# Performance work log

Measured on AMD Instinct MI355X. Metric: run time of the kernel, lower is better.

The kernel has to match this reference:

```python
import jax, jax.numpy as jnp
import numpy as np

N_NODES = 100000
N_EDGES = 1600000
HID = 128
HEADS = 8
DK = HID // HEADS
N_LAYERS = 4
IN_DIM = 32
N_CLASSES = 16


def _ln(x, g, b, eps=1e-5):
    mu = x.mean(-1, keepdims=True)
    var = x.var(-1, keepdims=True)
    return (x - mu) / jnp.sqrt(var + eps) * g + b


def setup_inputs() -> dict:
    key = jax.random.key(0)
    ks = jax.random.split(key, 24)
    s = 0.05
    inp = {
        'feat': jax.random.randint(ks[0], (N_NODES,), 0, IN_DIM, dtype=jnp.int32),
        'edge_src': jax.random.randint(ks[1], (N_EDGES,), 0, N_NODES, dtype=jnp.int32),
        'edge_dst': jnp.sort(jax.random.randint(ks[2], (N_EDGES,), 0, N_NODES, dtype=jnp.int32)),
        'emb': jax.random.normal(ks[3], (IN_DIM, HID), jnp.float32) * s,
        'Wq': jax.random.normal(ks[4], (N_LAYERS, HID, HID), jnp.float32) * s,
        'Wk': jax.random.normal(ks[5], (N_LAYERS, HID, HID), jnp.float32) * s,
        'Wv': jax.random.normal(ks[6], (N_LAYERS, HID, HID), jnp.float32) * s,
        'Wo': jax.random.normal(ks[7], (N_LAYERS, HID, HID), jnp.float32) * s,
        'bo': jnp.zeros((N_LAYERS, HID), jnp.float32),
        'ln1_g': jnp.ones((N_LAYERS, HID), jnp.float32),
        'ln1_b': jnp.zeros((N_LAYERS, HID), jnp.float32),
        'W1': jax.random.normal(ks[8], (N_LAYERS, HID, 2 * HID), jnp.float32) * s,
        'b1': jnp.zeros((N_LAYERS, 2 * HID), jnp.float32),
        'W2': jax.random.normal(ks[9], (N_LAYERS, 2 * HID, HID), jnp.float32) * s,
        'b2': jnp.zeros((N_LAYERS, HID), jnp.float32),
        'ln2_g': jnp.ones((N_LAYERS, HID), jnp.float32),
        'ln2_b': jnp.zeros((N_LAYERS, HID), jnp.float32),
        'mW0': jax.random.normal(ks[10], (HID, HID // 2), jnp.float32) * s,
        'mb0': jnp.zeros((HID // 2,), jnp.float32),
        'mW1': jax.random.normal(ks[11], (HID // 2, HID // 4), jnp.float32) * s,
        'mb1': jnp.zeros((HID // 4,), jnp.float32),
        'mW2': jax.random.normal(ks[12], (HID // 4, N_CLASSES), jnp.float32) * s,
        'mb2': jnp.zeros((N_CLASSES,), jnp.float32),
    }
    return inp


def reference(feat, edge_src, edge_dst, emb, Wq, Wk, Wv, Wo, bo, ln1_g, ln1_b,
              W1, b1, W2, b2, ln2_g, ln2_b, mW0, mb0, mW1, mb1, mW2, mb2):
    N = feat.shape[0]
    h = emb[feat]  # [N, HID] embedding gather
    inv_sqrt_dk = jnp.float32(1.0 / np.sqrt(DK))
    for l in range(Wq.shape[0]):
        h_in1 = h
        q = (h @ Wq[l]).reshape(N, HEADS, DK)
        k = (h @ Wk[l]).reshape(N, HEADS, DK)
        v = (h @ Wv[l]).reshape(N, HEADS, DK)
        # per-edge scores: K[src] . Q[dst], scaled, clipped, exponentiated
        sc = jnp.einsum('ehd,ehd->eh', k[edge_src], q[edge_dst]) * inv_sqrt_dk
        sc = jnp.exp(jnp.clip(sc, -5.0, 5.0))  # [E, HEADS]
        wV = jax.ops.segment_sum(sc[:, :, None] * v[edge_src], edge_dst, num_segments=N)
        z = jax.ops.segment_sum(sc, edge_dst, num_segments=N)
        attn = (wV / (z[:, :, None] + 1e-6)).reshape(N, HID)
        h = h_in1 + (attn @ Wo[l] + bo[l])  # residual + O proj
        h = _ln(h, ln1_g[l], ln1_b[l])
        h_in2 = h
        f = jax.nn.relu(h @ W1[l] + b1[l]) @ W2[l] + b2[l]
        h = _ln(h_in2 + f, ln2_g[l], ln2_b[l])
    # MLPReadout: HID -> HID/2 -> HID/4 -> n_classes
    h = jax.nn.relu(h @ mW0 + mb0)
    h = jax.nn.relu(h @ mW1 + mb1)
    return h @ mW2 + mb2
```

## Files before the change

### kernel.cpp

```cpp
#include <hip/hip_runtime.h>
#include <hip/hip_fp16.h>

#define HID 128
#define N_LAYERS 4
#define IN_DIM 32
#define N_CLASSES 16

typedef _Float16 f16x8 __attribute__((ext_vector_type(8)));
typedef float f32x2 __attribute__((ext_vector_type(2)));
typedef __attribute__((ext_vector_type(4))) float f32x4;
typedef unsigned int uint_t;

#if defined(__has_builtin)
#if __has_builtin(__builtin_amdgcn_cvt_pk_f32_fp8)
#define HAVE_CVT_FP8 1
#endif
#if __has_builtin(__builtin_amdgcn_cvt_pk_fp8_f32)
#define HAVE_ENC_FP8 1
#endif
#endif

__device__ __forceinline__ unsigned short f2bf(float f) {
    unsigned int u = __float_as_uint(f);
    return (unsigned short)((u + 0x7FFFu + ((u >> 16) & 1u)) >> 16);
}
__device__ __forceinline__ float2 up16(uint_t u) {
    __half2 h = *(__half2*)&u;
    return __half22float2(h);
}

__device__ __forceinline__ unsigned char f2e4m3(float f) {
    unsigned int u = __float_as_uint(f);
    unsigned char s = (unsigned char)((u >> 24) & 0x80u);
    unsigned int a = u & 0x7FFFFFFFu;
    if (a >= 0x43E00000u) return s | 0x7Eu;
    int exp = (int)(a >> 23) - 127;
    if (exp < -6) {
        int m = (int)rintf(__uint_as_float(a) * 512.f);
        return s | (unsigned char)m;
    }
    unsigned int lsb = (a >> 20) & 1u;
    a += 0x7FFFFu + lsb;
    int e8 = ((int)(a >> 23) - 127) + 7;
    unsigned int m8 = (a >> 20) & 7u;
    return s | (unsigned char)((e8 << 3) | (int)m8);
}
__device__ __forceinline__ float e4m32f(unsigned int b) {
    unsigned int s = (b & 0x80u) << 24;
    unsigned int E = (b >> 3) & 15u, m = b & 7u;
    if (E == 0) {
        float v = (float)m * 0.001953125f;
        return __uint_as_float(__float_as_uint(v) | s);
    }
    return __uint_as_float(s | ((E + 120u) << 23) | (m << 20));
}
__device__ __forceinline__ unsigned char enc8(float v) {
#ifdef HAVE_ENC_FP8
    int r = __builtin_amdgcn_cvt_pk_fp8_f32(v, v, 0, false);
    return (unsigned char)(r & 0xFF);
#else
    return f2e4m3(v);
#endif
}
__device__ __forceinline__ void dec8v(uint_t u, f32x2* o) {
#ifdef HAVE_CVT_FP8
    o[0] = __builtin_amdgcn_cvt_pk_f32_fp8(u, false);
    o[1] = __builtin_amdgcn_cvt_pk_f32_fp8(u, true);
#else
    o[0] = (f32x2){e4m32f(u & 255u), e4m32f((u >> 8) & 255u)};
    o[1] = (f32x2){e4m32f((u >> 16) & 255u), e4m32f(u >> 24)};
#endif
}

__device__ __forceinline__ int frag_off(int row, int c) {
    return ((c >> 5) << 10) + (((c >> 3) & 3) << 8) + (row << 4) + ((c & 7) << 1);
}

__global__ void detect_kernel(const unsigned int* __restrict__ ln1g, int* __restrict__ flag) {
    if (threadIdx.x == 0 && blockIdx.x == 0)
        *flag = (ln1g[0] == 0x3F800000u) ? 0 : 1;
}

#define NSM 11
struct SArgs {
    const void* src[NSM];
    float*      dst[NSM];
    int         cnt[NSM];
};

__global__ void conv_kernel(SArgs args, const int* __restrict__ flag) {
    int p = blockIdx.y;
    int n = args.cnt[p];
    int base = (blockIdx.x * 256 + threadIdx.x) * 4;
    if (base >= n) return;
    float* dst = args.dst[p];
    if (*flag) {
        const unsigned short* s = (const unsigned short*)args.src[p];
        #pragma unroll
        for (int j = 0; j < 4; ++j)
            dst[base + j] = __uint_as_float(((unsigned int)s[base + j]) << 16);
    } else {
        const float* s = (const float*)args.src[p];
        *(float4*)&dst[base] = *(const float4*)&s[base];
    }
}

#define NW 27
struct WArgs {
    const void* src[NW];
    int         soff[NW];
    _Float16*   dst[NW];
    int         K[NW];
    int         M[NW];
    int         mode[NW];
};

__global__ void wconv_kernel(WArgs a, const int* __restrict__ flag) {
    int p = blockIdx.y;
    int K = a.K[p], M = a.M[p], mode = a.mode[p];
    int idx = blockIdx.x * 256 + threadIdx.x;
    if (idx >= K * M) return;
    int k = idx / M, m = idx % M;
    float v;
    if (*flag)
        v = __uint_as_float(((unsigned int)((const unsigned short*)a.src[p])[a.soff[p] + idx]) << 16);
    else
        v = ((const float*)a.src[p])[a.soff[p] + idx];
    size_t off;
    if (mode == 0) {
        off = (size_t)m * K + k;
    } else {
        int ht, k2;
        if (mode == 1) { ht = m >> 5; k2 = k; }
        else           { ht = ((k >> 7) << 2) + (m >> 5); k2 = k & 127; }
        int frag = (((k2 >> 5) * 2 + ((m >> 4) & 1)) << 6) + (((k2 >> 3) & 3) << 4) + (m & 15);
        off = (size_t)ht * 4096 + frag * 8 + (k & 7);
    }
    a.dst[p][off] = (_Float16)v;
}

__global__ void csr_kernel(const int* __restrict__ dst, int* __restrict__ row_start,
                           int N, int E) {
    int n = blockIdx.x * 256 + threadIdx.x;
    if (n > N) return;
    int lo = 0, hi = E;
    while (lo < hi) {
        int mid = (lo + hi) >> 1;
        if (dst[mid] < n) lo = mid + 1; else hi = mid;
    }
    row_start[n] = lo;
}

__global__ void embed_kernel(const int* __restrict__ feat, const float* __restrict__ emb,
                             _Float16* __restrict__ h, int N) {
    int idx = blockIdx.x * 256 + threadIdx.x;
    if (idx >= N * 16) return;
    int n  = idx >> 4;
    int c8 = idx & 15;
    int f = feat[n];
    const float* s = &emb[(size_t)f * HID + c8 * 8];
    float4 a = *(const float4*)s;
    float4 b = *(const float4*)(s + 4);
    f16x8 o;
    o[0] = (_Float16)a.x; o[1] = (_Float16)a.y; o[2] = (_Float16)a.z; o[3] = (_Float16)a.w;
    o[4] = (_Float16)b.x; o[5] = (_Float16)b.y; o[6] = (_Float16)b.z; o[7] = (_Float16)b.w;
    *(f16x8*)&h[(size_t)n * HID + c8 * 8] = o;
}

__launch_bounds__(256)
__global__ void mfma_gemm_qkv(const _Float16* __restrict__ Ain,
                              const _Float16* __restrict__ Bt,
                              _Float16* __restrict__ q16, unsigned char* __restrict__ kvp8) {
    __shared__ __align__(16) char As[16384];
    __shared__ __align__(16) char Bs[49152];

    const int t    = threadIdx.x;
    const int w    = t >> 6;
    const int l    = t & 63;
    const int quad = l >> 4;
    const int lc   = l & 15;
    const int row0 = blockIdx.x * 64;
    const int mbase = blockIdx.y * 192;

    char* Aw = As + (w << 12);

    #pragma unroll
    for (int i = 0; i < 4; ++i) {
        int idx = i * 64 + l;
        int row = idx >> 4, g = idx & 15;
        uint4 v = *(const uint4*)(Ain + (size_t)(row0 + w * 16 + row) * 128 + g * 8);
        *(uint4*)(Aw + ((g >> 2) << 10) + ((g & 3) << 8) + (row << 4)) = v;
    }
    {
        const uint4* Bsrc = (const uint4*)(Bt + (size_t)(mbase / 32) * 4096);
        #pragma unroll
        for (int i = 0; i < 12; ++i) {
            int idx = t + i * 256;
            *(uint4*)&Bs[idx * 16] = Bsrc[idx];
        }
    }
    __syncthreads();

    f32x4 acc[12];
    #pragma unroll
    for (int i = 0; i < 12; ++i) acc[i] = (f32x4){0.f, 0.f, 0.f, 0.f};

    #pragma unroll
    for (int kk = 0; kk < 4; ++kk) {
        f16x8 af = *(const f16x8*)(Aw + (kk << 10) + (quad << 8) + (lc << 4));
        #pragma unroll
        for (int i = 0; i < 12; ++i) {
            f16x8 bf = *(const f16x8*)(Bs + (i >> 1) * 8192 +
                                       ((kk * 2 + (i & 1)) << 10) + (quad << 8) + (lc << 4));
            acc[i] = __builtin_amdgcn_mfma_f32_16x16x32_f16(af, bf, acc[i], 0, 0, 0);
        }
    }

    #pragma unroll
    for (int r = 0; r < 4; ++r) {
        int row = row0 + w * 16 + quad * 4 + r;
        #pragma unroll
        for (int i = 0; i < 12; ++i) {
            float v = acc[i][r];
            int gc = mbase + i * 16 + lc;
            if (gc < 128)      q16[(size_t)row * 128 + gc] = (_Float16)v;
            else if (gc < 256) kvp8[(size_t)row * 256 + (gc - 128)] = enc8(v);
            else               kvp8[(size_t)row * 256 + 128 + (gc - 256)] = enc8(v);
        }
    }
}

template<int NEXTM, bool RMODE>
__launch_bounds__(256, 3)
__global__ void layer_fused(_Float16* __restrict__ h,
                            const _Float16* __restrict__ Wo, const _Float16* __restrict__ W1,
                            const _Float16* __restrict__ W2,
                            const _Float16* __restrict__ Wn, const float* __restrict__ bn,
                            const float* __restrict__ bo,  const float* __restrict__ l1g,
                            const float* __restrict__ l1b, const float* __restrict__ b1,
                            const float* __restrict__ b2,  const float* __restrict__ l2g,
                            const float* __restrict__ l2b,
                            _Float16* __restrict__ q16,
                            const uint_t* __restrict__ kvin, unsigned char* __restrict__ kvout,
                            const int* __restrict__ esrc, const int* __restrict__ rows,
                            int N) {
    constexpr int NHT = NEXTM / 32;
    __shared__ __align__(16) char bufA[16384];
    __shared__ __align__(16) char bufH[16384];
    __shared__ __align__(16) char bufB[16384];

    const int t = threadIdx.x, w = t >> 6, l = t & 63;
    const int quad = l >> 4, lc = l & 15;
    const int row0 = blockIdx.x * 64;
    char* Aw = bufA + (w << 12);
    char* Hw = bufH + (w << 12);

    auto ISSUE = [&](const _Float16* src, int bsel) {
        char* d = bufB + bsel * 8192 + w * 2048;
        const char* g = (const char*)src + w * 2048 + l * 16;
        __builtin_amdgcn_global_load_lds(
            (const __attribute__((address_space(1))) unsigned int*)g,
            (__attribute__((address_space(3))) unsigned int*)d, 16, 0, 0);
        __builtin_amdgcn_global_load_lds(
            (const __attribute__((address_space(1))) unsigned int*)(g + 1024),
            (__attribute__((address_space(3))) unsigned int*)(d + 1024), 16, 0, 0);
    };
    auto MF2 = [&](const char* Ar, int bsel, f32x4* ac) {
        const char* B = bufB + bsel * 8192;
        #pragma unroll
        for (int kk = 0; kk < 4; ++kk) {
            f16x8 af = *(const f16x8*)(Ar + (kk << 10) + (quad << 8) + (lc << 4));
            #pragma unroll
            for (int i = 0; i < 2; ++i) {
                f16x8 bf = *(const f16x8*)(B + ((kk * 2 + i) << 10) + (quad << 8) + (lc << 4));
                ac[i] = __builtin_amdgcn_mfma_f32_16x16x32_f16(af, bf, ac[i], 0, 0, 0);
            }
        }
    };

    ISSUE(Wo, 0);

    _Float16 resv[4][8];
    #pragma unroll
    for (int r = 0; r < 4; ++r) {
        int row = row0 + w * 16 + quad * 4 + r;
        #pragma unroll
        for (int j = 0; j < 8; ++j)
            resv[r][j] = h[(size_t)row * 128 + j * 16 + lc];
    }

    {
        const int head = l & 7;
        const int rsub = l >> 3;
        #pragma unroll
        for (int task = 0; task < 2; ++task) {
            const int rr   = rsub + task * 8;
            const int node = row0 + w * 16 + rr;
            f16x8 o0, o1;
            #pragma unroll
            for (int j = 0; j < 8; ++j) { o0[j] = (_Float16)0; o1[j] = (_Float16)0; }
            if (node < N) {
                f32x2 qh[8];
                {
                    const uint4* qp = (const uint4*)(q16 + (size_t)node * HID + head * 16);
                    uint4 q0 = qp[0], q1 = qp[1];
                    uint_t qs[8] = {q0.x, q0.y, q0.z, q0.w, q1.x, q1.y, q1.z, q1.w};
                    #pragma unroll
                    for (int i = 0; i < 8; ++i) {
                        float2 f = up16(qs[i]);
                        qh[i] = (f32x2){f.x * 0.25f, f.y * 0.25f};
                    }
                }
                int e0 = rows[node], e1 = rows[node + 1];
                f32x2 wv[8];
                #pragma unroll
                for (int i = 0; i < 8; ++i) wv[i] = (f32x2){0.f, 0.f};
                float z = 0.f;

                uint4 ka = {0,0,0,0}, va = {0,0,0,0}, kc = {0,0,0,0}, vc = {0,0,0,0};
                bool oka = e0 < e1, okc = e0 + 1 < e1;
                if (oka) {
                    int sa = esrc[e0];
                    int sc = okc ? esrc[e0 + 1] : sa;
                    ka = *(const uint4*)(kvin + (size_t)sa * 64 + head * 4);
                    va = *(const uint4*)(kvin + (size_t)sa * 64 + 32 + head * 4);
                    kc = *(const uint4*)(kvin + (size_t)sc * 64 + head * 4);
                    vc = *(const uint4*)(kvin + (size_t)sc * 64 + 32 + head * 4);
                }
                for (int e = e0; e < e1; e += 2) {
                    uint4 cka = ka, cva = va, ckc = kc, cvc = vc;
                    bool coka = oka, cokc = okc;
                    int en = e + 2;
                    oka = en < e1; okc = en + 1 < e1;
                    if (oka) {
                        int sa = esrc[en];
                        int sc = okc ? esrc[en + 1] : sa;
                        ka = *(const uint4*)(kvin + (size_t)sa * 64 + head * 4);
                        va = *(const uint4*)(kvin + (size_t)sa * 64 + 32 + head * 4);
                        kc = *(const uint4*)(kvin + (size_t)sc * 64 + head * 4);
                        vc = *(const uint4*)(kvin + (size_t)sc * 64 + 32 + head * 4);
                    }
                    f32x2 k2a[8], k2c[8];
                    dec8v(cka.x, k2a); dec8v(cka.y, k2a + 2); dec8v(cka.z, k2a + 4); dec8v(cka.w, k2a + 6);
                    dec8v(ckc.x, k2c); dec8v(ckc.y, k2c + 2); dec8v(ckc.z, k2c + 4); dec8v(ckc.w, k2c + 6);
                    f32x2 da2 = (f32x2){0.f, 0.f}, dc2 = (f32x2){0.f, 0.f};
                    #pragma unroll
                    for (int j = 0; j < 8; ++j) { da2 += qh[j] * k2a[j]; dc2 += qh[j] * k2c[j]; }
                    float da = da2.x + da2.y, dc = dc2.x + dc2.y;
                    float sa2 = coka ? __expf(fminf(fmaxf(da, -5.f), 5.f)) : 0.f;
                    float sc2 = cokc ? __expf(fminf(fmaxf(dc, -5.f), 5.f)) : 0.f;

                    f32x2 v2a[8], v2c[8];
                    dec8v(cva.x, v2a); dec8v(cva.y, v2a + 2); dec8v(cva.z, v2a + 4); dec8v(cva.w, v2a + 6);
                    dec8v(cvc.x, v2c); dec8v(cvc.y, v2c + 2); dec8v(cvc.z, v2c + 4); dec8v(cvc.w, v2c + 6);
                    f32x2 pa = (f32x2){sa2, sa2}, pc = (f32x2){sc2, sc2};
                    #pragma unroll
                    for (int j = 0; j < 8; ++j) { wv[j] += pa * v2a[j]; wv[j] += pc * v2c[j]; }
                    z += sa2 + sc2;
                }
                float inv = 1.f / (z + 1e-6f);
                #pragma unroll
                for (int i = 0; i < 4; ++i) {
                    o0[2*i]   = (_Float16)(wv[i].x * inv);
                    o0[2*i+1] = (_Float16)(wv[i].y * inv);
                    o1[2*i]   = (_Float16)(wv[4+i].x * inv);
                    o1[2*i+1] = (_Float16)(wv[4+i].y * inv);
                }
            }
            *(f16x8*)(Aw + frag_off(rr, head * 16))     = o0;
            *(f16x8*)(Aw + frag_off(rr, head * 16 + 8)) = o1;
        }
    }

    __syncthreads();
    int bb = 0;

    f32x4 acc[8];
    #pragma unroll
    for (int i = 0; i < 8; ++i) acc[i] = (f32x4){0.f, 0.f, 0.f, 0.f};
    #pragma unroll
    for (int c = 0; c < 4; ++c) {
        ISSUE(c < 3 ? Wo + (c + 1) * 4096 : W1, bb ^ 1);
        MF2(Aw, bb, acc + c * 2);
        __syncthreads();
        bb ^= 1;
    }

    {
        float gv[8], bv[8], bb8[8];
        #pragma unroll
        for (int j = 0; j < 8; ++j) {
            int col = j * 16 + lc;
            gv[j] = l1g[col]; bv[j] = l1b[col]; bb8[j] = bo[col];
        }
        #pragma unroll
        for (int r = 0; r < 4; ++r) {
            float v[8];
            float s = 0.f, ss = 0.f;
            #pragma unroll
            for (int j = 0; j < 8; ++j) {
                v[j] = acc[j][r] + bb8[j] + (float)resv[r][j];
                s += v[j]; ss += v[j] * v[j];
            }
            #pragma unroll
            for (int m = 1; m <= 8; m <<= 1) { s += __shfl_xor(s, m); ss += __shfl_xor(ss, m); }
            float mu   = s * (1.f / 128.f);
            float rstd = rsqrtf(ss * (1.f / 128.f) - mu * mu + 1e-5f);
            #pragma unroll
            for (int j = 0; j < 8; ++j) {
                float o = (v[j] - mu) * rstd * gv[j] + bv[j];
                *(_Float16*)(Hw + frag_off(quad * 4 + r, j * 16 + lc)) = (_Float16)o;
            }
        }
    }

    f32x4 acc3[8];
    #pragma unroll
    for (int i = 0; i < 8; ++i) acc3[i] = (f32x4){0.f, 0.f, 0.f, 0.f};
    #pragma unroll
    for (int hh = 0; hh < 2; ++hh) {
        #pragma unroll
        for (int j = 0; j < 4; ++j) {
            ISSUE(j < 3 ? W1 + (hh * 4 + j + 1) * 4096 : W2 + (hh * 4) * 4096, bb ^ 1);
            f32x4 a2[2];
            a2[0] = (f32x4){0.f, 0.f, 0.f, 0.f};
            a2[1] = (f32x4){0.f, 0.f, 0.f, 0.f};
            MF2(Hw, bb, a2);
            #pragma unroll
            for (int r = 0; r < 4; ++r) {
                #pragma unroll
                for (int i2 = 0; i2 < 2; ++i2) {
                    float v = a2[i2][r] + b1[(hh * 4 + j) * 32 + i2 * 16 + lc];
                    v = fmaxf(v, 0.f);
                    *(_Float16*)(Aw + frag_off(quad * 4 + r, j * 32 + i2 * 16 + lc)) = (_Float16)v;
                }
            }
            __syncthreads();
            bb ^= 1;
        }
        #pragma unroll
        for (int j = 0; j < 4; ++j) {
            const _Float16* nxt;
            if (j < 3)          nxt = W2 + (hh * 4 + j + 1) * 4096;
            else if (hh == 0)   nxt = W1 + 4 * 4096;
            else                nxt = Wn;
            ISSUE(nxt, bb ^ 1);
            MF2(Aw, bb, acc3 + j * 2);
            __syncthreads();
            bb ^= 1;
        }
    }

    f16x8 ov[4];
    {
        float gv[8], bv[8], bb8[8];
        #pragma unroll
        for (int j = 0; j < 8; ++j) {
            int col = j * 16 + lc;
            gv[j] = l2g[col]; bv[j] = l2b[col]; bb8[j] = b2[col];
        }
        #pragma unroll
        for (int r = 0; r < 4; ++r) {
            float v[8];
            float s = 0.f, ss = 0.f;
            #pragma unroll
            for (int j = 0; j < 8; ++j) {
                float res = (float)*(const _Float16*)(Hw + frag_off(quad * 4 + r, j * 16 + lc));
                v[j] = acc3[j][r] + bb8[j] + res;
                s += v[j]; ss += v[j] * v[j];
            }
            #pragma unroll
            for (int m = 1; m <= 8; m <<= 1) { s += __shfl_xor(s, m); ss += __shfl_xor(ss, m); }
            float mu   = s * (1.f / 128.f);
            float rstd = rsqrtf(ss * (1.f / 128.f) - mu * mu + 1e-5f);
            #pragma unroll
            for (int j = 0; j < 8; ++j) {
                float o = (v[j] - mu) * rstd * gv[j] + bv[j];
                ov[r][j] = (_Float16)o;
                *(_Float16*)(Aw + frag_off(quad * 4 + r, j * 16 + lc)) = (_Float16)o;
            }
        }
    }

    auto storeP = [&](int p, const f32x4* pf) {
        #pragma unroll
        for (int r = 0; r < 4; ++r) {
            int row = row0 + w * 16 + quad * 4 + r;
            #pragma unroll
            for (int i2 = 0; i2 < 2; ++i2) {
                int gc = p * 32 + i2 * 16 + lc;
                float v = pf[i2][r];
                if (RMODE) {
                    v += bn[gc];
                    v = fmaxf(v, 0.f);
                    q16[(size_t)row * 64 + gc] = (_Float16)v;
                } else {
                    if (gc < 128)      q16[(size_t)row * 128 + gc] = (_Float16)v;
                    else if (gc < 256) kvout[(size_t)row * 256 + (gc - 128)] = enc8(v);
                    else               kvout[(size_t)row * 256 + 128 + (gc - 256)] = enc8(v);
                }
            }
        }
    };

    f32x4 pf[2];
    #pragma unroll
    for (int c = 0; c < NHT; ++c) {
        if (c + 1 < NHT) ISSUE(Wn + (c + 1) * 4096, bb ^ 1);
        if (c == 0) {
            #pragma unroll
            for (int r = 0; r < 4; ++r) {
                int row = row0 + w * 16 + quad * 4 + r;
                #pragma unroll
                for (int j = 0; j < 8; ++j)
                    h[(size_t)row * 128 + j * 16 + lc] = ov[r][j];
            }
        } else {
            storeP(c - 1, pf);
        }
        f32x4 a4[2];
        a4[0] = (f32x4){0.f, 0.f, 0.f, 0.f};
        a4[1] = (f32x4){0.f, 0.f, 0.f, 0.f};
        MF2(Aw, bb, a4);
        if (c + 1 < NHT) __syncthreads();
        bb ^= 1;
        pf[0] = a4[0]; pf[1] = a4[1];
    }
    storeP(NHT - 1, pf);
}

__launch_bounds__(256)
__global__ void readout_tail(const _Float16* __restrict__ r0,
                             const _Float16* __restrict__ w1t, const float* __restrict__ b1_,
                             const _Float16* __restrict__ w2t, const float* __restrict__ b2_,
                             void* __restrict__ outp, const int* __restrict__ flag, int N) {
    constexpr int SA = 144;
    constexpr int SR = 80;
    __shared__ __align__(16) char bufA[64 * SA];
    __shared__ __align__(16) char bufR[64 * SR];

    const int t    = threadIdx.x;
    const int w    = t >> 6;
    const int l    = t & 63;
    const int quad = l >> 4;
    const int lc   = l & 15;
    const int row0 = blockIdx.x * 64;

    #pragma unroll
    for (int i = 0; i < 2; ++i) {
        int idx = t + i * 256;
        int r = idx >> 3, u = idx & 7;
        *(uint4*)&bufA[r * SA + u * 16] = *(const uint4*)(r0 + (size_t)(row0 + r) * 64 + u * 8);
    }
    __syncthreads();

    f32x4 acc[2];
    acc[0] = (f32x4){0.f, 0.f, 0.f, 0.f};
    acc[1] = (f32x4){0.f, 0.f, 0.f, 0.f};
    #pragma unroll
    for (int kk = 0; kk < 2; ++kk) {
        f16x8 af = *(const f16x8*)&bufA[(w * 16 + lc) * SA + kk * 64 + quad * 16];
        #pragma unroll
        for (int i = 0; i < 2; ++i) {
            f16x8 bf = *(const f16x8*)(w1t + (size_t)(i * 16 + lc) * 64 + kk * 32 + quad * 8);
            acc[i] = __builtin_amdgcn_mfma_f32_16x16x32_f16(af, bf, acc[i], 0, 0, 0);
        }
    }
    #pragma unroll
    for (int r = 0; r < 4; ++r) {
        int lrow = (w * 16 + quad * 4 + r) * SR;
        #pragma unroll
        for (int i = 0; i < 2; ++i) {
            float v = acc[i][r] + b1_[i * 16 + lc];
            v = fmaxf(v, 0.f);
            *(_Float16*)&bufR[lrow + (i * 16 + lc) * 2] = (_Float16)v;
        }
    }
    __syncthreads();
    f32x4 a2 = (f32x4){0.f, 0.f, 0.f, 0.f};
    {
        f16x8 af = *(const f16x8*)&bufR[(w * 16 + lc) * SR + quad * 16];
        f16x8 bf = *(const f16x8*)(w2t + (size_t)lc * 32 + quad * 8);
        a2 = __builtin_amdgcn_mfma_f32_16x16x32_f16(af, bf, a2, 0, 0, 0);
    }
    #pragma unroll
    for (int r = 0; r < 4; ++r) {
        int row = row0 + w * 16 + quad * 4 + r;
        if (row < N) {
            float v = a2[r] + b2_[lc];
            size_t o = (size_t)row * 16 + lc;
            if (*flag) ((unsigned short*)outp)[o] = f2bf(v);
            else       ((float*)outp)[o] = v;
        }
    }
}

extern "C" void kernel_launch(void* const* d_in, const int* in_sizes, int n_in,
                              void* d_out, int out_size, void* d_ws, size_t ws_size,
                              hipStream_t stream) {
    const int N  = in_sizes[0];
    const int E  = in_sizes[1];
    const int RB = (N + 63) / 64;
    const size_t NP = (size_t)RB * 64;

    const int* d_feat = (const int*)d_in[0];
    const int* d_esrc = (const int*)d_in[1];
    const int* d_edst = (const int*)d_in[2];

    char* base = (char*)d_ws;
    size_t cur = 0;
    auto alloc = [&](size_t bytes) -> char* {
        cur = (cur + 255) & ~(size_t)255;
        char* p = base + cur;
        cur += bytes;
        return p;
    };
    int* d_flag = (int*)alloc(4);
    int* d_rows = (int*)alloc((size_t)(N + 1) * 4);

    float* p_emb = (float*)alloc(IN_DIM * HID * 4);
    float* p_bo  = (float*)alloc(N_LAYERS * HID * 4);
    float* p_l1g = (float*)alloc(N_LAYERS * HID * 4);
    float* p_l1b = (float*)alloc(N_LAYERS * HID * 4);
    float* p_b1  = (float*)alloc(N_LAYERS * 2 * HID * 4);
    float* p_b2  = (float*)alloc(N_LAYERS * HID * 4);
    float* p_l2g = (float*)alloc(N_LAYERS * HID * 4);
    float* p_l2b = (float*)alloc(N_LAYERS * HID * 4);
    float* p_mb0 = (float*)alloc(64 * 4);
    float* p_mb1 = (float*)alloc(32 * 4);
    float* p_mb2 = (float*)alloc(16 * 4);

    _Float16* wqkv_t = (_Float16*)alloc((size_t)N_LAYERS * 384 * 128 * 2);
    _Float16* wo_t   = (_Float16*)alloc((size_t)N_LAYERS * 128 * 128 * 2);
    _Float16* w1_t   = (_Float16*)alloc((size_t)N_LAYERS * 256 * 128 * 2);
    _Float16* w2_t   = (_Float16*)alloc((size_t)N_LAYERS * 128 * 256 * 2);
    _Float16* mw0_t  = (_Float16*)alloc(64 * 128 * 2);
    _Float16* mw1_t  = (_Float16*)alloc(32 * 64 * 2);
    _Float16* mw2_t  = (_Float16*)alloc(16 * 32 * 2);

    _Float16*      buf_h = (_Float16*)alloc(NP * HID * 2);
    _Float16*      q16   = (_Float16*)alloc(NP * HID * 2);
    unsigned char* kv0   = (unsigned char*)alloc(NP * 256);
    unsigned char* kv1   = (unsigned char*)alloc(NP * 256);

    detect_kernel<<<1, 64, 0, stream>>>((const unsigned int*)d_in[9], d_flag);

    {
        SArgs sa;
        const int sidx[NSM] = {3, 8, 9, 10, 12, 14, 15, 16, 18, 20, 22};
        float*    sdst[NSM] = {p_emb, p_bo, p_l1g, p_l1b, p_b1, p_b2, p_l2g, p_l2b, p_mb0, p_mb1, p_mb2};
        const int scnt[NSM] = {IN_DIM*HID, N_LAYERS*HID, N_LAYERS*HID, N_LAYERS*HID,
                               N_LAYERS*2*HID, N_LAYERS*HID, N_LAYERS*HID, N_LAYERS*HID, 64, 32, 16};
        for (int i = 0; i < NSM; ++i) { sa.src[i] = d_in[sidx[i]]; sa.dst[i] = sdst[i]; sa.cnt[i] = scnt[i]; }
        conv_kernel<<<dim3(4, NSM), 256, 0, stream>>>(sa, d_flag);
    }

    {
        WArgs wa;
        int wi = 0;
        auto addw = [&](int inp, int off, int Kd, int Md, _Float16* dst, int mode) {
            wa.src[wi] = d_in[inp]; wa.soff[wi] = off; wa.K[wi] = Kd; wa.M[wi] = Md;
            wa.dst[wi] = dst; wa.mode[wi] = mode; ++wi;
        };
        for (int l = 0; l < N_LAYERS; ++l) {
            addw(4,  l * 16384, 128, 128, wqkv_t + (size_t)l * 49152, 1);
            addw(5,  l * 16384, 128, 128, wqkv_t + (size_t)l * 49152 + 16384, 1);
            addw(6,  l * 16384, 128, 128, wqkv_t + (size_t)l * 49152 + 32768, 1);
            addw(7,  l * 16384, 128, 128, wo_t + (size_t)l * 16384, 1);
            addw(11, l * 32768, 128, 256, w1_t + (size_t)l * 32768, 1);
            addw(13, l * 32768, 256, 128, w2_t + (size_t)l * 32768, 2);
        }
        addw(17, 0, 128, 64, mw0_t, 1);
        addw(19, 0, 64,  32, mw1_t, 0);
        addw(21, 0, 32,  16, mw2_t, 0);
        wconv_kernel<<<dim3(128, NW), 256, 0, stream>>>(wa, d_flag);
    }

    csr_kernel<<<(N + 1 + 255) / 256, 256, 0, stream>>>(d_edst, d_rows, N, E);
    embed_kernel<<<((size_t)N * 16 + 255) / 256, 256, 0, stream>>>(d_feat, p_emb, buf_h, N);

    mfma_gemm_qkv<<<dim3(RB, 2), 256, 0, stream>>>(buf_h, wqkv_t, q16, kv0);

    for (int l = 0; l < N_LAYERS; ++l) {
        const _Float16* Wo = wo_t + (size_t)l * 16384;
        const _Float16* W1 = w1_t + (size_t)l * 32768;
        const _Float16* W2 = w2_t + (size_t)l * 32768;
        const float* bo  = p_bo  + (size_t)l * HID;
        const float* l1g = p_l1g + (size_t)l * HID;
        const float* l1b = p_l1b + (size_t)l * HID;
        const float* b1  = p_b1  + (size_t)l * 2 * HID;
        const float* b2  = p_b2  + (size_t)l * HID;
        const float* l2g = p_l2g + (size_t)l * HID;
        const float* l2b = p_l2b + (size_t)l * HID;

        const uint_t*  kvin  = (const uint_t*)((l & 1) ? kv1 : kv0);
        unsigned char* kvout = (l & 1) ? kv0 : kv1;

        if (l < N_LAYERS - 1) {
            layer_fused<384, false><<<RB, 256, 0, stream>>>(
                buf_h, Wo, W1, W2, wqkv_t + (size_t)(l + 1) * 49152, nullptr,
                bo, l1g, l1b, b1, b2, l2g, l2b, q16, kvin, kvout, d_esrc, d_rows, N);
        } else {
            layer_fused<64, true><<<RB, 256, 0, stream>>>(
                buf_h, Wo, W1, W2, mw0_t, p_mb0,
                bo, l1g, l1b, b1, b2, l2g, l2b, q16, kvin, kvout, d_esrc, d_rows, N);
        }
    }

    readout_tail<<<RB, 256, 0, stream>>>(q16, mw1_t, p_mb1, mw2_t, p_mb2, d_out, d_flag, N);
}
```

Baseline: 744.1 us.

## Read weight fragments directly from global memory instead of staging through LDS

Drops the double-buffered LDS weight staging (global_load_lds plus a __syncthreads per 32-column chunk) from the fused layer kernel. Each wave now loads B fragments straight from global/L2 and keeps its A fragments in registers via LDA. This frees 16 KB of LDS and removes block barriers, and occupancy is raised to 4 blocks per CU. The cost is redundant weight reads per wave from cache and possible register pressure. The readout intermediate row stride also changes from 64 to 128.

Measured after the change: 906.8 us. 1.22x slower.

```diff
diff --git a/kernel.cpp b/kernel.cpp
--- a/kernel.cpp
+++ b/kernel.cpp
@@ -231,7 +231,7 @@
 }
 
 template<int NEXTM, bool RMODE>
-__launch_bounds__(256, 3)
+__launch_bounds__(256, 4)
 __global__ void layer_fused(_Float16* __restrict__ h,
                             const _Float16* __restrict__ Wo, const _Float16* __restrict__ W1,
                             const _Float16* __restrict__ W2,
@@ -247,7 +247,6 @@
     constexpr int NHT = NEXTM / 32;
     __shared__ __align__(16) char bufA[16384];
     __shared__ __align__(16) char bufH[16384];
-    __shared__ __align__(16) char bufB[16384];
 
     const int t = threadIdx.x, w = t >> 6, l = t & 63;
     const int quad = l >> 4, lc = l & 15;
@@ -255,30 +254,22 @@
     char* Aw = bufA + (w << 12);
     char* Hw = bufH + (w << 12);
 
-    auto ISSUE = [&](const _Float16* src, int bsel) {
-        char* d = bufB + bsel * 8192 + w * 2048;
-        const char* g = (const char*)src + w * 2048 + l * 16;
-        __builtin_amdgcn_global_load_lds(
-            (const __attribute__((address_space(1))) unsigned int*)g,
-            (__attribute__((address_space(3))) unsigned int*)d, 16, 0, 0);
-        __builtin_amdgcn_global_load_lds(
-            (const __attribute__((address_space(1))) unsigned int*)(g + 1024),
-            (__attribute__((address_space(3))) unsigned int*)(d + 1024), 16, 0, 0);
+    auto LDA = [&](const char* Ar, f16x8* afc) {
+        #pragma unroll
+        for (int kk = 0; kk < 4; ++kk)
+            afc[kk] = *(const f16x8*)(Ar + (kk << 10) + (quad << 8) + (lc << 4));
     };
-    auto MF2 = [&](const char* Ar, int bsel, f32x4* ac) {
-        const char* B = bufB + bsel * 8192;
+    auto MF2G = [&](const f16x8* afc, const _Float16* B, f32x4* ac) {
         #pragma unroll
         for (int kk = 0; kk < 4; ++kk) {
-            f16x8 af = *(const f16x8*)(Ar + (kk << 10) + (quad << 8) + (lc << 4));
             #pragma unroll
             for (int i = 0; i < 2; ++i) {
-                f16x8 bf = *(const f16x8*)(B + ((kk * 2 + i) << 10) + (quad << 8) + (lc << 4));
-                ac[i] = __builtin_amdgcn_mfma_f32_16x16x32_f16(af, bf, ac[i], 0, 0, 0);
+                f16x8 bf = *(const f16x8*)((const char*)B +
+                            (((kk * 2 + i) << 10) + (quad << 8) + (lc << 4)));
+                ac[i] = __builtin_amdgcn_mfma_f32_16x16x32_f16(afc[kk], bf, ac[i], 0, 0, 0);
             }
         }
     };
-
-    ISSUE(Wo, 0);
 
     _Float16 resv[4][8];
     #pragma unroll
@@ -372,19 +363,14 @@
         }
     }
 
-    __syncthreads();
-    int bb = 0;
-
+    f16x8 afc[4];
+    LDA(Aw, afc);
     f32x4 acc[8];
     #pragma unroll
     for (int i = 0; i < 8; ++i) acc[i] = (f32x4){0.f, 0.f, 0.f, 0.f};
     #pragma unroll
-    for (int c = 0; c < 4; ++c) {
-        ISSUE(c < 3 ? Wo + (c + 1) * 4096 : W1, bb ^ 1);
-        MF2(Aw, bb, acc + c * 2);
-        __syncthreads();
-        bb ^= 1;
-    }
+    for (int c = 0; c < 4; ++c)
+        MF2G(afc, Wo + (size_t)c * 4096, acc + c * 2);
 
     {
         float gv[8], bv[8], bb8[8];
@@ -417,15 +403,16 @@
     f32x4 acc3[8];
     #pragma unroll
     for (int i = 0; i < 8; ++i) acc3[i] = (f32x4){0.f, 0.f, 0.f, 0.f};
+    f16x8 afh[4];
+    LDA(Hw, afh);
     #pragma unroll
     for (int hh = 0; hh < 2; ++hh) {
         #pragma unroll
         for (int j = 0; j < 4; ++j) {
-            ISSUE(j < 3 ? W1 + (hh * 4 + j + 1) * 4096 : W2 + (hh * 4) * 4096, bb ^ 1);
             f32x4 a2[2];
             a2[0] = (f32x4){0.f, 0.f, 0.f, 0.f};
             a2[1] = (f32x4){0.f, 0.f, 0.f, 0.f};
-            MF2(Hw, bb, a2);
+            MF2G(afh, W1 + (size_t)(hh * 4 + j) * 4096, a2);
             #pragma unroll
             for (int r = 0; r < 4; ++r) {
                 #pragma unroll
@@ -435,23 +422,14 @@
                     *(_Float16*)(Aw + frag_off(quad * 4 + r, j * 32 + i2 * 16 + lc)) = (_Float16)v;
                 }
             }
-            __syncthreads();
-            bb ^= 1;
-        }
-        #pragma unroll
-        for (int j = 0; j < 4; ++j) {
-            const _Float16* nxt;
-            if (j < 3)          nxt = W2 + (hh * 4 + j + 1) * 4096;
-            else if (hh == 0)   nxt = W1 + 4 * 4096;
-            else                nxt = Wn;
-            ISSUE(nxt, bb ^ 1);
-            MF2(Aw, bb, acc3 + j * 2);
-            __syncthreads();
-            bb ^= 1;
-        }
-    }
-
-    f16x8 ov[4];
+        }
+        f16x8 aft[4];
+        LDA(Aw, aft);
+        #pragma unroll
+        for (int j = 0; j < 4; ++j)
+            MF2G(aft, W2 + (size_t)(hh * 4 + j) * 4096, acc3 + j * 2);
+    }
+
     {
         float gv[8], bv[8], bb8[8];
         #pragma unroll
@@ -461,6 +439,7 @@
         }
         #pragma unroll
         for (int r = 0; r < 4; ++r) {
+            int row = row0 + w * 16 + quad * 4 + r;
             float v[8];
             float s = 0.f, ss = 0.f;
             #pragma unroll
@@ -476,24 +455,30 @@
             #pragma unroll
             for (int j = 0; j < 8; ++j) {
                 float o = (v[j] - mu) * rstd * gv[j] + bv[j];
-                ov[r][j] = (_Float16)o;
+                h[(size_t)row * 128 + j * 16 + lc] = (_Float16)o;
                 *(_Float16*)(Aw + frag_off(quad * 4 + r, j * 16 + lc)) = (_Float16)o;
             }
         }
     }
 
-    auto storeP = [&](int p, const f32x4* pf) {
+    LDA(Aw, afc);
+    #pragma unroll
+    for (int c = 0; c < NHT; ++c) {
+        f32x4 a4[2];
+        a4[0] = (f32x4){0.f, 0.f, 0.f, 0.f};
+        a4[1] = (f32x4){0.f, 0.f, 0.f, 0.f};
+        MF2G(afc, Wn + (size_t)c * 4096, a4);
         #pragma unroll
         for (int r = 0; r < 4; ++r) {
             int row = row0 + w * 16 + quad * 4 + r;
             #pragma unroll
             for (int i2 = 0; i2 < 2; ++i2) {
-                int gc = p * 32 + i2 * 16 + lc;
-                float v = pf[i2][r];
+                int gc = c * 32 + i2 * 16 + lc;
+                float v = a4[i2][r];
                 if (RMODE) {
                     v += bn[gc];
                     v = fmaxf(v, 0.f);
-                    q16[(size_t)row * 64 + gc] = (_Float16)v;
+                    q16[(size_t)row * 128 + gc] = (_Float16)v;
                 } else {
                     if (gc < 128)      q16[(size_t)row * 128 + gc] = (_Float16)v;
                     else if (gc < 256) kvout[(size_t)row * 256 + (gc - 128)] = enc8(v);
@@ -501,32 +486,7 @@
                 }
             }
         }
-    };
-
-    f32x4 pf[2];
-    #pragma unroll
-    for (int c = 0; c < NHT; ++c) {
-        if (c + 1 < NHT) ISSUE(Wn + (c + 1) * 4096, bb ^ 1);
-        if (c == 0) {
-            #pragma unroll
-            for (int r = 0; r < 4; ++r) {
-                int row = row0 + w * 16 + quad * 4 + r;
-                #pragma unroll
-                for (int j = 0; j < 8; ++j)
-                    h[(size_t)row * 128 + j * 16 + lc] = ov[r][j];
-            }
-        } else {
-            storeP(c - 1, pf);
-        }
-        f32x4 a4[2];
-        a4[0] = (f32x4){0.f, 0.f, 0.f, 0.f};
-        a4[1] = (f32x4){0.f, 0.f, 0.f, 0.f};
-        MF2(Aw, bb, a4);
-        if (c + 1 < NHT) __syncthreads();
-        bb ^= 1;
-        pf[0] = a4[0]; pf[1] = a4[1];
-    }
-    storeP(NHT - 1, pf);
+    }
 }
 
 __launch_bounds__(256)
@@ -550,7 +510,7 @@
     for (int i = 0; i < 2; ++i) {
         int idx = t + i * 256;
         int r = idx >> 3, u = idx & 7;
-        *(uint4*)&bufA[r * SA + u * 16] = *(const uint4*)(r0 + (size_t)(row0 + r) * 64 + u * 8);
+        *(uint4*)&bufA[r * SA + u * 16] = *(const uint4*)(r0 + (size_t)(row0 + r) * 128 + u * 8);
     }
     __syncthreads();
 
```
